# Performance work log

Hardware: AMD Instinct MI355X
Metric: run time of the kernel (lower is better)

The kernel has to match this reference:

```python
import jax, jax.numpy as jnp
import numpy as np


def _pairwise_euclidean(features):
    # [N, N] Euclidean distances with a grad-safe sqrt at the zero diagonal.
    sq_norms = jnp.sum(features * features, axis=1)
    sq = sq_norms[:, None] + sq_norms[None, :] - 2.0 * (features @ features.T)
    sq = jnp.maximum(sq, 0.0)
    safe = jnp.where(sq > 0.0, sq, 1.0)
    return jnp.where(sq > 0.0, jnp.sqrt(safe), 0.0)


def setup_inputs() -> dict:
    key = jax.random.key(0)
    k1, k2 = jax.random.split(key)
    N, D = 8192, 512
    features = jax.random.normal(k1, (N, D), dtype=jnp.float32)
    adjacency_matrix = jax.random.uniform(k2, (N, N), dtype=jnp.float32)
    return {"features": features, "adjacency_matrix": adjacency_matrix, "num_neighbors": 8}


def reference(features, adjacency_matrix, num_neighbors):
    # Vectorized build_adj_hypergraph_glo:
    # per-row: normalize_tensor(adj[i]) + normalize_tensor(||f[i] - f||), then topk(k+1)
    N = features.shape[0]
    adj_norm = adjacency_matrix / jnp.sum(adjacency_matrix, axis=1, keepdims=True)
    eud = _pairwise_euclidean(features)
    eud_norm = eud / jnp.sum(eud, axis=1, keepdims=True)
    distances = adj_norm + eud_norm                     # [N, N]
    # torch.topk defaults to largest=True -> faithful: take the k+1 largest
    vals, idx = jax.lax.top_k(distances, num_neighbors + 1)  # [N, k+1]
    src = jnp.repeat(jnp.arange(N, dtype=jnp.int32), num_neighbors + 1)
    edge_index = jnp.stack([src, idx.reshape(-1).astype(jnp.int32)], axis=0)  # [2, N*(k+1)]
    edge_weights = vals.reshape(-1)                     # [N*(k+1)]
    return edge_index, edge_weights
```

## Files before the change

### kernel.cpp

```cpp
#include <hip/hip_runtime.h>
#include <hip/hip_bf16.h>
#include <math.h>


typedef short bf16x8 __attribute__((ext_vector_type(8)));
typedef float f32x4 __attribute__((ext_vector_type(4)));

__device__ __forceinline__ float fbar(float x) {
  asm volatile("" : "+v"(x));
  return x;
}
__device__ __forceinline__ unsigned short f2bf(float x) {
  union { float f; unsigned u; } v; v.f = x;
  unsigned r = (v.u + 0x7fffu + ((v.u >> 16) & 1u)) >> 16;
  return (unsigned short)r;
}
__device__ __forceinline__ float bf2f(unsigned short b) {
  union { unsigned u; float f; } v; v.u = ((unsigned)b) << 16; return v.f;
}

__global__ __launch_bounds__(256) void knn_cvt(const float* __restrict__ f,
                                               unsigned short* __restrict__ hi,
                                               unsigned short* __restrict__ lo,
                                               int n4) {
  int i = blockIdx.x * 256 + threadIdx.x;
  if (i >= n4) return;
  float4 v = ((const float4*)f)[i];
  ushort4 h, l;
  h.x = f2bf(v.x); l.x = f2bf(v.x - bf2f(h.x));
  h.y = f2bf(v.y); l.y = f2bf(v.y - bf2f(h.y));
  h.z = f2bf(v.z); l.z = f2bf(v.z - bf2f(h.z));
  h.w = f2bf(v.w); l.w = f2bf(v.w - bf2f(h.w));
  ((ushort4*)hi)[i] = h;
  ((ushort4*)lo)[i] = l;
}

__global__ __launch_bounds__(128) void knn_sqn_np(const float* __restrict__ f,
                                                  float* __restrict__ sqn32,
                                                  int N, int D) {
  int row = blockIdx.x;
  int t = threadIdx.x;
  __shared__ float a[512];
  __shared__ float R[4][8];
  const float* fr = f + (size_t)row * D;
  float4 v = ((const float4*)fr)[t];
  a[t * 4 + 0] = v.x * v.x;
  a[t * 4 + 1] = v.y * v.y;
  a[t * 4 + 2] = v.z * v.z;
  a[t * 4 + 3] = v.w * v.w;
  __syncthreads();
  if (t < 32) {
    int lf = t >> 3, m = t & 7;
    float s = a[lf * 128 + m];
    for (int g = 1; g < 16; ++g) s += a[lf * 128 + 8 * g + m];
    R[lf][m] = s;
  }
  __syncthreads();
  if (t == 0) {
    float L[4];
#pragma unroll
    for (int lf = 0; lf < 4; ++lf)
      L[lf] = ((R[lf][0] + R[lf][1]) + (R[lf][2] + R[lf][3])) +
              ((R[lf][4] + R[lf][5]) + (R[lf][6] + R[lf][7]));
    sqn32[row] = (L[0] + L[1]) + (L[2] + L[3]);
  }
}

#define TBM 128
#define TBN 128
#define TBK 32
__global__ __launch_bounds__(256) void knn_gemm_mfma(
    const unsigned short* __restrict__ fhi, const unsigned short* __restrict__ flo,
    const float* __restrict__ sqn32, unsigned short* __restrict__ eud,
    float* __restrict__ leaf, int N, int D) {
  __shared__ __align__(16) char smem[40960];
  unsigned short (*Ah)[40] = (unsigned short(*)[40])(smem);
  unsigned short (*Al)[40] = (unsigned short(*)[40])(smem + 10240);
  unsigned short (*Bh)[40] = (unsigned short(*)[40])(smem + 20480);
  unsigned short (*Bl)[40] = (unsigned short(*)[40])(smem + 30720);

  int tid = threadIdx.x;

  int NT = N / TBM;
  int b = blockIdx.x;
  int by = 0, rem = NT;
  while (b >= rem) { b -= rem; ++by; --rem; }
  int bx = by + b;

  int i0 = by * TBM, j0 = bx * TBN;
  int wid = tid >> 6, l = tid & 63;
  int wr = wid >> 1, wc = wid & 1;
  int lr = l & 15, lk = l >> 4;

  f32x4 acc[4][4] = {};

  int sr = tid >> 1;
  int sh = (tid & 1) << 4;

  for (int k0 = 0; k0 < D; k0 += TBK) {
    size_t aoff = (size_t)(i0 + sr) * D + k0 + sh;
    size_t boff = (size_t)(j0 + sr) * D + k0 + sh;
    *(uint4*)&Ah[sr][sh]     = *(const uint4*)(fhi + aoff);
    *(uint4*)&Ah[sr][sh + 8] = *(const uint4*)(fhi + aoff + 8);
    *(uint4*)&Al[sr][sh]     = *(const uint4*)(flo + aoff);
    *(uint4*)&Al[sr][sh + 8] = *(const uint4*)(flo + aoff + 8);
    *(uint4*)&Bh[sr][sh]     = *(const uint4*)(fhi + boff);
    *(uint4*)&Bh[sr][sh + 8] = *(const uint4*)(fhi + boff + 8);
    *(uint4*)&Bl[sr][sh]     = *(const uint4*)(flo + boff);
    *(uint4*)&Bl[sr][sh + 8] = *(const uint4*)(flo + boff + 8);
    __syncthreads();

    bf16x8 ah[4], al_[4], bh[4], bl_[4];
#pragma unroll
    for (int fr = 0; fr < 4; ++fr) {
      ah[fr]  = *(const bf16x8*)&Ah[wr * 64 + fr * 16 + lr][lk * 8];
      al_[fr] = *(const bf16x8*)&Al[wr * 64 + fr * 16 + lr][lk * 8];
      bh[fr]  = *(const bf16x8*)&Bh[wc * 64 + fr * 16 + lr][lk * 8];
      bl_[fr] = *(const bf16x8*)&Bl[wc * 64 + fr * 16 + lr][lk * 8];
    }
#pragma unroll
    for (int fr = 0; fr < 4; ++fr)
#pragma unroll
      for (int fc = 0; fc < 4; ++fc) {
        acc[fr][fc] = __builtin_amdgcn_mfma_f32_16x16x32_bf16(
            ah[fr], bh[fc], acc[fr][fc], 0, 0, 0);
        acc[fr][fc] = __builtin_amdgcn_mfma_f32_16x16x32_bf16(
            ah[fr], bl_[fc], acc[fr][fc], 0, 0, 0);
        acc[fr][fc] = __builtin_amdgcn_mfma_f32_16x16x32_bf16(
            al_[fr], bh[fc], acc[fr][fc], 0, 0, 0);
      }
    __syncthreads();
  }

  float (*Et)[132] = (float(*)[132])(smem);
  float (*R2)[8]   = (float(*)[8])(smem + 33792);
  float (*R3)[8]   = (float(*)[8])(smem + 35840);

  float sj[4];
#pragma unroll
  for (int fc = 0; fc < 4; ++fc) sj[fc] = sqn32[j0 + wc * 64 + fc * 16 + lr];

  bool mir = (bx != by);

#pragma unroll
  for (int pass = 0; pass < 2; ++pass) {
    if (wr == pass) {
#pragma unroll
      for (int fr = 0; fr < 4; ++fr) {
#pragma unroll
        for (int v = 0; v < 4; ++v) {
          int irow = fr * 16 + lk * 4 + v;
          int i = i0 + pass * 64 + irow;
          float si = sqn32[i];
#pragma unroll
          for (int fc = 0; fc < 4; ++fc) {
            int jcol = wc * 64 + fc * 16 + lr;
            int j = j0 + jcol;
            float sq = si + sj[fc] - 2.0f * acc[fr][fc][v];
            float e = (sq > 0.0f && i != j) ? sqrtf(sq) : 0.0f;
            Et[irow][jcol] = e;
            int q = (int)(e * 1024.0f + 0.5f);
            if (q > 65535) q = 65535;
            eud[(size_t)i * N + j] = (unsigned short)q;
          }
        }
      }
    }
    __syncthreads();

#pragma unroll
    for (int u0 = 0; u0 < 2; ++u0) {
      int u = tid + u0 * 256;
      int row = u >> 3, m = u & 7;
      float s = Et[row][m];
#pragma unroll
      for (int g = 1; g < 16; ++g) s += Et[row][8 * g + m];
      R2[row][m] = s;
    }

    if (mir) {
#pragma unroll
      for (int u0 = 0; u0 < 4; ++u0) {
        int u = tid + u0 * 256;
        int jofs = u >> 3, m = u & 7;
        float s = (pass == 0) ? 0.0f : R3[jofs][m];
#pragma unroll
        for (int g = 0; g < 8; ++g) s += Et[8 * g + m][jofs];
        R3[jofs][m] = s;
      }
      {
        int j = tid >> 1, h = tid & 1;
        size_t base = (size_t)(j0 + j) * N + i0 + pass * 64 + h * 32;
        unsigned short buf[32];
#pragma unroll
        for (int ii = 0; ii < 32; ++ii) {
          float e = Et[h * 32 + ii][j];
          int q = (int)(e * 1024.0f + 0.5f);
          if (q > 65535) q = 65535;
          buf[ii] = (unsigned short)q;
        }
#pragma unroll
        for (int q4 = 0; q4 < 4; ++q4)
          *(uint4*)(eud + base + q4 * 8) = *(uint4*)&buf[q4 * 8];
      }
    }
    __syncthreads();

    if (tid < 64) {
      float v = ((R2[tid][0] + R2[tid][1]) + (R2[tid][2] + R2[tid][3])) +
                ((R2[tid][4] + R2[tid][5]) + (R2[tid][6] + R2[tid][7]));
      leaf[(size_t)(i0 + pass * 64 + tid) * 64 + bx] = v;
    }
    if (mir && pass == 1 && tid < 128) {
      float v = ((R3[tid][0] + R3[tid][1]) + (R3[tid][2] + R3[tid][3])) +
                ((R3[tid][4] + R3[tid][5]) + (R3[tid][6] + R3[tid][7]));
      leaf[(size_t)(j0 + tid) * 64 + by] = v;
    }
    __syncthreads();
  }
}

#define SWP(a, b, ia, ib) { float _t = a; a = b; b = _t; int _q = ia; ia = ib; ib = _q; }
#define INS(s, jj)                                        \
  if ((s) > v7) {                                         \
    v7 = (s); x7 = (jj);                                  \
    if (v7 > v6) SWP(v6, v7, x6, x7)                      \
    if (v6 > v5) SWP(v5, v6, x5, x6)                      \
    if (v5 > v4) SWP(v4, v5, x4, x5)                      \
    if (v4 > v3) SWP(v3, v4, x3, x4)                      \
    if (v3 > v2) SWP(v2, v3, x2, x3)                      \
    if (v2 > v1) SWP(v1, v2, x1, x2)                      \
    if (v1 > v0) SWP(v0, v1, x0, x1)                      \
  }

__global__ __launch_bounds__(256) void knn_rowsel(
    const float* __restrict__ adj, const unsigned short* __restrict__ eud,
    const float* __restrict__ leaf, int* __restrict__ cand,
    float* __restrict__ cansc,
    float* __restrict__ SaOut, float* __restrict__ SeOut, int N) {
  __shared__ float arow[8192];
  __shared__ float R[64][8];
  __shared__ float Lf[64];
  __shared__ float bc[2];
  int row = blockIdx.x;
  int t = threadIdx.x;
  const float* ar = adj + (size_t)row * N;

#pragma unroll
  for (int c = 0; c < 8; ++c)
    ((float4*)arow)[c * 256 + t] = ((const float4*)ar)[c * 256 + t];
  __syncthreads();

  for (int u = t; u < 512; u += 256) {
    int lf = u >> 3, m = u & 7;
    float s = arow[lf * 128 + m];
    for (int g = 1; g < 16; ++g) s += arow[lf * 128 + 8 * g + m];
    R[lf][m] = s;
  }
  __syncthreads();
  if (t < 64)
    Lf[t] = ((R[t][0] + R[t][1]) + (R[t][2] + R[t][3])) +
            ((R[t][4] + R[t][5]) + (R[t][6] + R[t][7]));
  __syncthreads();
  for (int w = 32; w >= 1; w >>= 1) {
    if (t < w) Lf[t] = Lf[2 * t] + Lf[2 * t + 1];
    __syncthreads();
  }
  if (t == 0) { float Sa = Lf[0]; SaOut[row] = Sa; bc[0] = 1.0f / Sa; }
  __syncthreads();

  if (t < 64) Lf[t] = leaf[(size_t)row * 64 + t];
  __syncthreads();
  for (int w = 32; w >= 1; w >>= 1) {
    if (t < w) Lf[t] = Lf[2 * t] + Lf[2 * t + 1];
    __syncthreads();
  }
  if (t == 0) {
    float Se = Lf[0]; SeOut[row] = Se;
    bc[1] = (float)(1.0 / ((double)Se * 1024.0));
  }
  __syncthreads();
  float ra = bc[0], re = bc[1];

  const unsigned short* er = eud + (size_t)row * N;
  float v0 = -3.0e38f, v1 = -3.0e38f, v2 = -3.0e38f, v3 = -3.0e38f;
  float v4 = -3.0e38f, v5 = -3.0e38f, v6 = -3.0e38f, v7 = -3.0e38f;
  int x0 = 0, x1 = 0, x2 = 0, x3 = 0, x4 = 0, x5 = 0, x6 = 0, x7 = 0;
#pragma unroll
  for (int it = 0; it < 8; ++it) {
    int j = it * 1024 + t * 4;
    float4 av = *(const float4*)(arow + j);
    ushort4 ev = *(const ushort4*)(er + j);
    float s0 = av.x * ra + (float)ev.x * re;
    float s1 = av.y * ra + (float)ev.y * re;
    float s2 = av.z * ra + (float)ev.z * re;
    float s3 = av.w * ra + (float)ev.w * re;
    INS(s0, j + 0)
    INS(s1, j + 1)
    INS(s2, j + 2)
    INS(s3, j + 3)
  }

  int lane = t & 63, wv = t >> 6;
  int* cw = cand + (size_t)row * 64 + wv * 16;
  float* csw = cansc + (size_t)row * 64 + wv * 16;
#pragma unroll
  for (int sel = 0; sel < 16; ++sel) {
    float cv = v0; int cj = x0;
    for (int off = 32; off; off >>= 1) {
      float ov = __shfl_xor(cv, off);
      int oj = __shfl_xor(cj, off);
      if (ov > cv || (ov == cv && oj < cj)) { cv = ov; cj = oj; }
    }
    if (lane == 0) { cw[sel] = cj; csw[sel] = cv; }
    if (v0 == cv && x0 == cj) {
      v0 = v1; x0 = x1; v1 = v2; x1 = x2; v2 = v3; x2 = x3; v3 = v4; x3 = x4;
      v4 = v5; x4 = x5; v5 = v6; x5 = x6; v6 = v7; x6 = x7;
      v7 = -3.0e38f; x7 = 0x7fffffff;
    }
  }
}

__global__ __launch_bounds__(256) void knn_refine(
    const float* __restrict__ f, const float* __restrict__ adj,
    const float* __restrict__ Sa, const float* __restrict__ Se,
    const int* __restrict__ cand, const float* __restrict__ cansc,
    float* __restrict__ out, int N, int D, int KP1) {
  int row = blockIdx.x;
  int t = threadIdx.x;
  int wave = t >> 6, lane = t & 63;

  __shared__ float fis[4][136];
  __shared__ float fjs[4][2][4][136];
  __shared__ float sval[64];
  __shared__ float asc[64];
  __shared__ int   ajx[64];
  __shared__ int   gidx[16];

  if (t < 64) {
    ajx[t] = cand[(size_t)row * 64 + t];
    asc[t] = cansc[(size_t)row * 64 + t];
    sval[t] = -3.0e38f;
  }
  if (t < 128) {
    int e0 = t * 4;
    *(float4*)&fis[e0 >> 7][e0 & 127] =
        ((const float4*)(f + (size_t)row * D))[t];
  }
  __syncthreads();

  if (t < 64) {
    int myj = ajx[t]; float mys = asc[t];
    int rank = 0;
    for (int c = 0; c < 64; ++c) {
      float v = asc[c]; int jc = ajx[c];
      if (v > mys || (v == mys && jc < myj)) ++rank;
    }
    if (rank < 16) gidx[rank] = t;
  }
  __syncthreads();

  float sa = Sa[row], se = Se[row];
  int h = lane >> 5;
  int hl = lane & 31;
  int lf = hl >> 3, m = hl & 7;

#pragma unroll
  for (int p = 0; p < 2; ++p) {
    int slot = wave * 4 + p * 2 + h;
    int c = gidx[slot];
    int j = ajx[c];

    const float4* fj4 = (const float4*)(f + (size_t)j * D);
#pragma unroll
    for (int q = 0; q < 4; ++q) {
      int e0 = (hl * 4 + q) * 4;
      *(float4*)&fjs[wave][h][e0 >> 7][e0 & 127] = fj4[hl * 4 + q];
    }

    const float* ai = fis[lf];
    const float* bi = fjs[wave][h][lf];
    float d0 = ai[m] - bi[m];
    float acc = fbar(d0 * d0);
#pragma unroll
    for (int g = 1; g < 16; ++g) {
      float d = ai[8 * g + m] - bi[8 * g + m];
      acc = acc + fbar(d * d);
    }
    float u = acc + __shfl_xor(acc, 1);
    u = u + __shfl_xor(u, 2);
    u = u + __shfl_xor(u, 4);
    float s1 = u + __shfl_xor(u, 8);
    float sq = s1 + __shfl_xor(s1, 16);

    if (hl == 0) {
      float e = sq > 0.0f ? (float)sqrt((double)sq) : 0.0f;
      sval[c] = adj[(size_t)row * N + j] / sa + e / se;
    }
  }
  __syncthreads();

  if (wave == 0) {
    float v = sval[lane];
    int j = ajx[lane];
    size_t NK = (size_t)N * KP1;
    size_t ob = (size_t)row * KP1;
    for (int r = 0; r < KP1; ++r) {
      float cv = v; int cj = j;
      for (int off = 32; off; off >>= 1) {
        float ov = __shfl_xor(cv, off);
        int oj = __shfl_xor(cj, off);
        if (ov > cv || (ov == cv && oj < cj)) { cv = ov; cj = oj; }
      }
      if (lane == 0) {
        out[ob + r]          = (float)row;
        out[NK + ob + r]     = (float)cj;
        out[2 * NK + ob + r] = cv;
      }
      if (j == cj) v = -2.0f;
    }
  }
}

static inline size_t alignup(size_t x, size_t a) { return (x + a - 1) & ~(a - 1); }

extern "C" void kernel_launch(void* const* d_in, const int* in_sizes, int n_in,
                              void* d_out, int out_size, void* d_ws, size_t ws_size,
                              hipStream_t stream) {
  const float* f   = (const float*)d_in[0];
  const float* adj = (const float*)d_in[1];

  long long nn = in_sizes[1];
  int N = (int)llround(sqrt((double)nn));
  int D = in_sizes[0] / N;
  int KP1 = out_size / (3 * N);

  char* w = (char*)d_ws;
  size_t off = 0;
  float* sqn32 = (float*)(w + off); off = alignup(off + (size_t)N * 4, 256);
  float* Sa    = (float*)(w + off); off = alignup(off + (size_t)N * 4, 256);
  float* Se    = (float*)(w + off); off = alignup(off + (size_t)N * 4, 256);
  float* leaf  = (float*)(w + off); off = alignup(off + (size_t)N * 64 * 4, 256);
  int* cand    = (int*)(w + off);   off = alignup(off + (size_t)N * 64 * 4, 256);
  float* cansc = (float*)(w + off); off = alignup(off + (size_t)N * 64 * 4, 256);
  unsigned short* fhi = (unsigned short*)(w + off); off = alignup(off + (size_t)N * D * 2, 256);
  unsigned short* flo = (unsigned short*)(w + off); off = alignup(off + (size_t)N * D * 2, 256);
  unsigned short* eud = (unsigned short*)(w + off); off += (size_t)N * N * 2;
  (void)ws_size;

  int n4 = N * D / 4;
  int NT = N / TBM;
  int nblk = NT * (NT + 1) / 2;
  knn_cvt<<<(n4 + 255) / 256, 256, 0, stream>>>(f, fhi, flo, n4);
  knn_sqn_np<<<N, 128, 0, stream>>>(f, sqn32, N, D);
  knn_gemm_mfma<<<nblk, 256, 0, stream>>>(fhi, flo, sqn32, eud, leaf, N, D);
  knn_rowsel<<<N, 256, 0, stream>>>(adj, eud, leaf, cand, cansc, Sa, Se, N);
  knn_refine<<<N, 256, 0, stream>>>(f, adj, Sa, Se, cand, cansc,
                                    (float*)d_out, N, D, KP1);
}
```

Before: 461.8 us.

## Replace per-thread top-8 insertion with threshold filter and shared-memory candidate selection

The row-select kernel no longer keeps a per-thread sorted top-8 list and merges four waves' lists with shuffles. It first computes per-thread maxima and takes the 16th-largest of those as a threshold. It then recomputes the scores, appends values at or above the threshold into a shared list through atomics, and one wave picks the top 16 from that list. This drops the branchy insertion network, but it adds a second pass over the row, shared atomics and a serial 16-round selection. It also changes the candidate layout from 64 to 16 real candidates per row, with the remaining slots padded.

```diff
diff --git a/kernel.cpp b/kernel.cpp
--- a/kernel.cpp
+++ b/kernel.cpp
@@ -220,19 +220,6 @@
   }
 }
 
-#define SWP(a, b, ia, ib) { float _t = a; a = b; b = _t; int _q = ia; ia = ib; ib = _q; }
-#define INS(s, jj)                                        \
-  if ((s) > v7) {                                         \
-    v7 = (s); x7 = (jj);                                  \
-    if (v7 > v6) SWP(v6, v7, x6, x7)                      \
-    if (v6 > v5) SWP(v5, v6, x5, x6)                      \
-    if (v5 > v4) SWP(v4, v5, x4, x5)                      \
-    if (v4 > v3) SWP(v3, v4, x3, x4)                      \
-    if (v3 > v2) SWP(v2, v3, x2, x3)                      \
-    if (v2 > v1) SWP(v1, v2, x1, x2)                      \
-    if (v1 > v0) SWP(v0, v1, x0, x1)                      \
-  }
-
 __global__ __launch_bounds__(256) void knn_rowsel(
     const float* __restrict__ adj, const unsigned short* __restrict__ eud,
     const float* __restrict__ leaf, int* __restrict__ cand,
@@ -242,6 +229,12 @@
   __shared__ float R[64][8];
   __shared__ float Lf[64];
   __shared__ float bc[2];
+  __shared__ float maxv[256];
+  __shared__ float tauS;
+  __shared__ int   cnt;
+  __shared__ float ls[2048];
+  __shared__ int   lj[2048];
+
   int row = blockIdx.x;
   int t = threadIdx.x;
   const float* ar = adj + (size_t)row * N;
@@ -249,6 +242,7 @@
 #pragma unroll
   for (int c = 0; c < 8; ++c)
     ((float4*)arow)[c * 256 + t] = ((const float4*)ar)[c * 256 + t];
+  if (t == 0) cnt = 0;
   __syncthreads();
 
   for (int u = t; u < 512; u += 256) {
@@ -283,9 +277,38 @@
   float ra = bc[0], re = bc[1];
 
   const unsigned short* er = eud + (size_t)row * N;
-  float v0 = -3.0e38f, v1 = -3.0e38f, v2 = -3.0e38f, v3 = -3.0e38f;
-  float v4 = -3.0e38f, v5 = -3.0e38f, v6 = -3.0e38f, v7 = -3.0e38f;
-  int x0 = 0, x1 = 0, x2 = 0, x3 = 0, x4 = 0, x5 = 0, x6 = 0, x7 = 0;
+
+  float mx = -3.0e38f;
+#pragma unroll
+  for (int it = 0; it < 8; ++it) {
+    int j = it * 1024 + t * 4;
+    float4 av = *(const float4*)(arow + j);
+    ushort4 ev = *(const ushort4*)(er + j);
+    mx = fmaxf(mx, av.x * ra + (float)ev.x * re);
+    mx = fmaxf(mx, av.y * ra + (float)ev.y * re);
+    mx = fmaxf(mx, av.z * ra + (float)ev.z * re);
+    mx = fmaxf(mx, av.w * ra + (float)ev.w * re);
+  }
+  maxv[t] = mx;
+  __syncthreads();
+
+  if (t < 64) {
+    float a0 = maxv[t], a1 = maxv[t + 64], a2 = maxv[t + 128], a3 = maxv[t + 192];
+#pragma unroll
+    for (int r = 0; r < 16; ++r) {
+      float lm = fmaxf(fmaxf(a0, a1), fmaxf(a2, a3));
+      float cv = lm;
+      for (int off = 32; off; off >>= 1) cv = fmaxf(cv, __shfl_xor(cv, off));
+      if (r == 15 && t == 0) tauS = cv;
+      if (a0 == cv) a0 = -3.0e38f;
+      if (a1 == cv) a1 = -3.0e38f;
+      if (a2 == cv) a2 = -3.0e38f;
+      if (a3 == cv) a3 = -3.0e38f;
+    }
+  }
+  __syncthreads();
+  float tau = tauS;
+
 #pragma unroll
   for (int it = 0; it < 8; ++it) {
     int j = it * 1024 + t * 4;
@@ -295,28 +318,39 @@
     float s1 = av.y * ra + (float)ev.y * re;
     float s2 = av.z * ra + (float)ev.z * re;
     float s3 = av.w * ra + (float)ev.w * re;
-    INS(s0, j + 0)
-    INS(s1, j + 1)
-    INS(s2, j + 2)
-    INS(s3, j + 3)
-  }
-
-  int lane = t & 63, wv = t >> 6;
-  int* cw = cand + (size_t)row * 64 + wv * 16;
-  float* csw = cansc + (size_t)row * 64 + wv * 16;
-#pragma unroll
-  for (int sel = 0; sel < 16; ++sel) {
-    float cv = v0; int cj = x0;
-    for (int off = 32; off; off >>= 1) {
-      float ov = __shfl_xor(cv, off);
-      int oj = __shfl_xor(cj, off);
-      if (ov > cv || (ov == cv && oj < cj)) { cv = ov; cj = oj; }
-    }
-    if (lane == 0) { cw[sel] = cj; csw[sel] = cv; }
-    if (v0 == cv && x0 == cj) {
-      v0 = v1; x0 = x1; v1 = v2; x1 = x2; v2 = v3; x2 = x3; v3 = v4; x3 = x4;
-      v4 = v5; x4 = x5; v5 = v6; x5 = x6; v6 = v7; x6 = x7;
-      v7 = -3.0e38f; x7 = 0x7fffffff;
+    if (s0 >= tau) { int p = atomicAdd(&cnt, 1); if (p < 2048) { ls[p] = s0; lj[p] = j + 0; } }
+    if (s1 >= tau) { int p = atomicAdd(&cnt, 1); if (p < 2048) { ls[p] = s1; lj[p] = j + 1; } }
+    if (s2 >= tau) { int p = atomicAdd(&cnt, 1); if (p < 2048) { ls[p] = s2; lj[p] = j + 2; } }
+    if (s3 >= tau) { int p = atomicAdd(&cnt, 1); if (p < 2048) { ls[p] = s3; lj[p] = j + 3; } }
+  }
+  __syncthreads();
+  int C = cnt < 2048 ? cnt : 2048;
+
+  if (t >= 16 && t < 64) {
+    cand[(size_t)row * 64 + t] = 0x40000000 + t;
+    cansc[(size_t)row * 64 + t] = -3.0e38f;
+  }
+
+  if (t < 64) {
+    for (int r = 0; r < 16; ++r) {
+      float bv = -3.0e38f; int bj = 0x7fffffff; int bp = -1;
+      for (int i = t; i < C; i += 64) {
+        float v = ls[i]; int jj = lj[i];
+        if (v > bv || (v == bv && jj < bj)) { bv = v; bj = jj; bp = i; }
+      }
+      for (int off = 32; off; off >>= 1) {
+        float ov = __shfl_xor(bv, off);
+        int oj = __shfl_xor(bj, off);
+        int op = __shfl_xor(bp, off);
+        if (ov > bv || (ov == bv && oj < bj)) { bv = ov; bj = oj; bp = op; }
+      }
+      if (t == 0) {
+        cand[(size_t)row * 64 + r] = bj;
+        cansc[(size_t)row * 64 + r] = bv;
+        ls[bp] = -3.0e38f;
+      }
+      asm volatile("s_waitcnt lgkmcnt(0)" ::: "memory");
+      __builtin_amdgcn_sched_barrier(0);
     }
   }
 }
```

New measurement: 518.6 us. +12.3%, slower.
